# Kernel tuning notes

Hardware: AMD Instinct MI355X
Metric: run time of the kernel (lower is better)

Reference implementation:

```python
import jax, jax.numpy as jnp
import numpy as np

B, T, D = 2, 4096, 768
H = 12
HD = D // H  # 64
SCALE = 1.0 / np.sqrt(HD)


def setup_inputs() -> dict:
    key = jax.random.key(0)
    k1, k2, k3 = jax.random.split(key, 3)
    x = jax.random.normal(k1, (B, T, D), dtype=jnp.float32)
    W_qkv = jax.random.normal(k2, (D, 3 * D), dtype=jnp.float32) * (1.0 / np.sqrt(D))
    b_qkv = jnp.zeros((3 * D,), dtype=jnp.float32)
    W_out = jax.random.normal(k3, (D, D), dtype=jnp.float32) * (1.0 / np.sqrt(D))
    b_out = jnp.zeros((D,), dtype=jnp.float32)
    return {"x": x, "W_qkv": W_qkv, "b_qkv": b_qkv, "W_out": W_out, "b_out": b_out}


def reference(x, W_qkv, b_qkv, W_out, b_out):
    Bx, Tx, C = x.shape
    qkv = x @ W_qkv + b_qkv                                  # [B,T,3D]
    qkv = qkv.reshape(Bx, Tx, 3, H, HD).transpose(2, 0, 3, 1, 4)  # [3,B,H,T,hd]
    q, k, v = qkv[0], qkv[1], qkv[2]
    scores = jnp.einsum('bhqd,bhkd->bhqk', q, k) * SCALE      # [B,H,T,T]
    causal = jnp.tril(jnp.ones((Tx, Tx), dtype=bool))
    scores = jnp.where(causal[None, None], scores, -jnp.inf)
    attn = jax.nn.softmax(scores, axis=-1)
    out = jnp.einsum('bhqk,bhkd->bhqd', attn, v)              # [B,H,T,hd]
    out = out.transpose(0, 2, 1, 3).reshape(Bx, Tx, C)        # [B,T,D]
    return out @ W_out + b_out
```

## Files before the change

kernel.cpp:

```cpp
#include <hip/hip_runtime.h>
#include <cstdint>
#include <cstddef>

typedef _Float16 f16x8 __attribute__((ext_vector_type(8)));
typedef _Float16 f16x4 __attribute__((ext_vector_type(4)));
typedef float    f32x4 __attribute__((ext_vector_type(4)));

#define AS_GLOBAL __attribute__((address_space(1)))
#define AS_LDS    __attribute__((address_space(3)))

__device__ __forceinline__ void load16_to_lds(const _Float16* g, _Float16* l) {
    __builtin_amdgcn_global_load_lds((const AS_GLOBAL void*)g, (AS_LDS void*)l, 16, 0, 0);
}

#define BB   2
#define TT   4096
#define DD   768
#define NH   12
#define HDIM 64
#define D3   2304
#define SC2  (0.125f * 1.44269504088896f)

__global__ __launch_bounds__(256) void prep(const float* __restrict__ x,
                                            _Float16* __restrict__ Xh,
                                            const float* __restrict__ Wqkv,
                                            _Float16* __restrict__ Wqkvt,
                                            const float* __restrict__ Wout,
                                            _Float16* __restrict__ Wot) {
    const int bid = blockIdx.x, tid = threadIdx.x;
    if (bid < 6144) {
        const int i = bid * 1024 + tid * 4;
        float4 v = *(const float4*)(x + i);
        f16x4 h;
        h[0] = (_Float16)v.x; h[1] = (_Float16)v.y;
        h[2] = (_Float16)v.z; h[3] = (_Float16)v.w;
        *(f16x4*)(Xh + i) = h;
        return;
    }
    __shared__ float tile[32][33];
    const float* in; _Float16* out; int C, bx, by;
    if (bid < 7872) {
        const int t = bid - 6144;
        in = Wqkv; out = Wqkvt; C = 2304;
        bx = (t % 72) * 32; by = (t / 72) * 32;
    } else {
        const int t = bid - 7872;
        in = Wout; out = Wot; C = 768;
        bx = (t % 24) * 32; by = (t / 24) * 32;
    }
    const int R = 768;
    const int tx = tid & 31, ty = tid >> 5;
#pragma unroll
    for (int j = 0; j < 32; j += 8)
        tile[ty + j][tx] = in[(size_t)(by + ty + j) * C + bx + tx];
    __syncthreads();
#pragma unroll
    for (int j = 0; j < 32; j += 8)
        out[(size_t)(bx + ty + j) * R + by + tx] = (_Float16)tile[tx][ty + j];
}

template <typename OutT>
__device__ __forceinline__ void gemm_body(const _Float16* __restrict__ A,
                                          const _Float16* __restrict__ Bt,
                                          const float* __restrict__ bias, bool bias_row,
                                          OutT* __restrict__ C, int N, int K,
                                          int m0, int n0,
                                          _Float16* As, _Float16* Bs) {
    const int tid  = threadIdx.x;
    const int wave = tid >> 6, lane = tid & 63, quad = lane >> 4, l16 = lane & 15;
    const int wm = (wave & 1) * 64, wn = (wave >> 1) * 64;
    const int rowc = lane >> 3, part = lane & 7;

    f32x4 acc[4][4];
#pragma unroll
    for (int i = 0; i < 4; ++i)
#pragma unroll
        for (int n = 0; n < 4; ++n) acc[i][n] = f32x4{0.f, 0.f, 0.f, 0.f};

    for (int k0 = 0; k0 < K; k0 += 64) {
        __syncthreads();
#pragma unroll
        for (int cc = 0; cc < 4; ++cc) {
            const int ch = wave * 4 + cc;
            load16_to_lds(A  + (size_t)(m0 + ch * 8 + rowc) * K + k0 + part * 8,
                          As + ch * 512);
            load16_to_lds(Bt + (size_t)(n0 + ch * 8 + rowc) * K + k0 + part * 8,
                          Bs + ch * 512);
        }
        __syncthreads();
#pragma unroll
        for (int i = 0; i < 4; ++i) {
            f16x8 a0 = *(const f16x8*)(As + (wm + i * 16 + l16) * 64 + quad * 8);
            f16x8 a1 = *(const f16x8*)(As + (wm + i * 16 + l16) * 64 + 32 + quad * 8);
#pragma unroll
            for (int n = 0; n < 4; ++n) {
                f16x8 b0 = *(const f16x8*)(Bs + (wn + n * 16 + l16) * 64 + quad * 8);
                f16x8 b1 = *(const f16x8*)(Bs + (wn + n * 16 + l16) * 64 + 32 + quad * 8);
                acc[i][n] = __builtin_amdgcn_mfma_f32_16x16x32_f16(a0, b0, acc[i][n], 0, 0, 0);
                acc[i][n] = __builtin_amdgcn_mfma_f32_16x16x32_f16(a1, b1, acc[i][n], 0, 0, 0);
            }
        }
    }
#pragma unroll
    for (int i = 0; i < 4; ++i)
#pragma unroll
        for (int n = 0; n < 4; ++n)
#pragma unroll
            for (int r = 0; r < 4; ++r) {
                const int row = m0 + wm + i * 16 + quad * 4 + r;
                const int col = n0 + wn + n * 16 + l16;
                const float bv = bias_row ? bias[row] : bias[col];
                C[(size_t)row * N + col] = (OutT)(acc[i][n][r] + bv);
            }
}

__global__ __launch_bounds__(256) void gemm_qkv(const _Float16* __restrict__ Xh,
                                                const _Float16* __restrict__ Wqkvt,
                                                const float* __restrict__ bqkv,
                                                _Float16* __restrict__ QKh,
                                                _Float16* __restrict__ VtG) {
    __shared__ __align__(16) _Float16 As[128 * 64];
    __shared__ __align__(16) _Float16 Bs[128 * 64];
    const int bid = blockIdx.x;
    if (bid < 768) {
        const int bx = bid % 12, by = bid / 12;
        gemm_body<_Float16>(Xh, Wqkvt, bqkv, false, QKh, 1536, DD,
                            by * 128, bx * 128, As, Bs);
    } else {
        const int t = bid - 768;
        const int bx = t % 64, by = t / 64;
        gemm_body<_Float16>(Wqkvt + (size_t)1536 * DD, Xh, bqkv + 1536, true, VtG,
                            8192, DD, by * 128, bx * 128, As, Bs);
    }
}

__global__ __launch_bounds__(256) void gemm_out(const _Float16* __restrict__ A,
                                                const _Float16* __restrict__ Bt,
                                                const float* __restrict__ bias,
                                                float* __restrict__ C) {
    __shared__ __align__(16) _Float16 As[128 * 64];
    __shared__ __align__(16) _Float16 Bs[128 * 64];
    gemm_body<float>(A, Bt, bias, false, C, DD, DD,
                     (int)blockIdx.y * 128, (int)blockIdx.x * 128, As, Bs);
}

__global__ __launch_bounds__(256) void attn_kernel(const _Float16* __restrict__ qk,
                                                   const _Float16* __restrict__ vt,
                                                   _Float16* __restrict__ ao) {
    __shared__ __align__(16) _Float16 Ks[2][64 * 64];
    __shared__ __align__(16) _Float16 Vs[2][64 * 64];
    __shared__ __align__(16) _Float16 Ps[2][4][16 * 64];

    const int L    = blockIdx.x;
    const int xcd  = L & 7;
    const int r_   = L >> 3;
    const int gIdx = r_ >> 5;
    const int x    = r_ & 31;
    const int g    = gIdx * 8 + xcd;
    const int b = g / NH, h = g % NH;

    const int tid = threadIdx.x;
    const int wave = tid >> 6, lane = tid & 63, quad = lane >> 4, l16 = lane & 15;

    f16x8 ones;
#pragma unroll
    for (int j = 0; j < 8; ++j) ones[j] = (_Float16)1.0f;

    int vK[2], vV[2];
#pragma unroll
    for (int p = 0; p < 2; ++p) {
        const int j  = wave * 16 + p * 8 + (lane >> 3);
        const int sig = (j & 15) * 4 + (j >> 4);
        const int cdk = (lane & 7) ^ (j & 7);
        vK[p] = (b * TT + sig) * 1536 + DD + h * HDIM + cdk * 8;
        vV[p] = (h * HDIM + j) * 8192 + b * TT + cdk * 8;
    }
    auto stageK = [&](int buf, int k0) {
        const int kK = k0 * 1536;
#pragma unroll
        for (int p = 0; p < 2; ++p)
            load16_to_lds(qk + (vK[p] + kK), Ks[buf] + (wave * 16 + p * 8) * 64);
    };
    auto stageV = [&](int buf, int k0) {
#pragma unroll
        for (int p = 0; p < 2; ++p)
            load16_to_lds(vt + (vV[p] + k0), Vs[buf] + (wave * 16 + p * 8) * 64);
    };

    _Float16* const PsW = &Ps[0][wave][0];
    int pwo[4];
#pragma unroll
    for (int r = 0; r < 4; ++r) {
        const int row = quad * 4 + r;
        pwo[r] = row * 64 + (((l16 >> 1) ^ (row & 7)) * 8) + (l16 & 1) * 4;
    }
    int pro[2];
#pragma unroll
    for (int kh = 0; kh < 2; ++kh)
        pro[kh] = l16 * 64 + (((kh * 4 + quad) ^ (l16 & 7)) * 8);

    auto process = [&](int qt) {
        const int q0 = qt * 64;
        const int nkt = qt + 1;
        const int qrow = q0 + wave * 16 + quad * 4;
        f16x8 aq[2];
        {
            const int qoff = (b * TT + q0 + wave * 16 + l16) * 1536 + h * HDIM + quad * 8;
            const _Float16 sc = (_Float16)SC2;
            aq[0] = *(const f16x8*)(qk + qoff) * sc;
            aq[1] = *(const f16x8*)(qk + qoff + 32) * sc;
        }
        f32x4 o[4], lac;
#pragma unroll
        for (int n = 0; n < 4; ++n) o[n] = f32x4{0.f, 0.f, 0.f, 0.f};
        lac = f32x4{0.f, 0.f, 0.f, 0.f};

        auto pv = [&](int pbuf, int vbuf) {
#pragma unroll
            for (int kh = 0; kh < 2; ++kh) {
                f16x8 ap = *(const f16x8*)(PsW + pbuf * 4096 + pro[kh]);
                lac = __builtin_amdgcn_mfma_f32_16x16x32_f16(ap, ones, lac, 0, 0, 0);
#pragma unroll
                for (int n = 0; n < 4; ++n) {
                    const int posv = (kh * 4 + quad) ^ (l16 & 7);
                    f16x8 bv = *(const f16x8*)(Vs[vbuf] + (n * 16 + l16) * 64 + posv * 8);
                    o[n] = __builtin_amdgcn_mfma_f32_16x16x32_f16(ap, bv, o[n], 0, 0, 0);
                }
            }
        };

        __syncthreads();
        stageK(0, 0);
        int cur = 0;
        for (int kt = 0; kt < nkt; ++kt) {
            __syncthreads();
            if (kt + 1 < nkt) stageK(cur ^ 1, (kt + 1) * 64);
            stageV(cur, kt * 64);

            __builtin_amdgcn_s_setprio(1);
            f32x4 s[4];
#pragma unroll
            for (int n = 0; n < 4; ++n) s[n] = f32x4{0.f, 0.f, 0.f, 0.f};
#pragma unroll
            for (int kh = 0; kh < 2; ++kh)
#pragma unroll
                for (int n = 0; n < 4; ++n) {
                    const int pos = (kh * 4 + quad) ^ (l16 & 7);
                    f16x8 bk = *(const f16x8*)(Ks[cur] + (n * 16 + l16) * 64 + pos * 8);
                    s[n] = __builtin_amdgcn_mfma_f32_16x16x32_f16(aq[kh], bk, s[n], 0, 0, 0);
                }

            if (kt > 0) pv(cur ^ 1, cur ^ 1);
            __builtin_amdgcn_s_setprio(0);

            if (kt == nkt - 1) {
#pragma unroll
                for (int n = 0; n < 4; ++n) {
                    const int kg = kt * 64 + l16 * 4 + n;
#pragma unroll
                    for (int r = 0; r < 4; ++r)
                        if (kg > qrow + r) s[n][r] = -1e30f;
                }
            }

#pragma unroll
            for (int r = 0; r < 4; ++r) {
                f16x4 pk;
#pragma unroll
                for (int n = 0; n < 4; ++n)
                    pk[n] = (_Float16)__builtin_amdgcn_exp2f(s[n][r]);
                *(f16x4*)(PsW + cur * 4096 + pwo[r]) = pk;
            }
            cur ^= 1;
        }

        __syncthreads();
        pv(cur ^ 1, cur ^ 1);

#pragma unroll
        for (int r = 0; r < 4; ++r) {
            const float inv = 1.0f / lac[r];
            const int ooff = (b * TT + qrow + r) * DD + h * HDIM + l16;
#pragma unroll
            for (int n = 0; n < 4; ++n)
                ao[ooff + n * 16] = (_Float16)(o[n][r] * inv);
        }
    };

    process(63 - x);
    process(x);
}

extern "C" void kernel_launch(void* const* d_in, const int* in_sizes, int n_in,
                              void* d_out, int out_size, void* d_ws, size_t ws_size,
                              hipStream_t stream) {
    const float* x     = (const float*)d_in[0];
    const float* Wqkv  = (const float*)d_in[1];
    const float* bqkv  = (const float*)d_in[2];
    const float* Wout  = (const float*)d_in[3];
    const float* bout  = (const float*)d_in[4];
    float* out = (float*)d_out;

    char* ws = (char*)d_ws;
    _Float16* Xh    = (_Float16*)ws;  ws += (size_t)BB * TT * DD * 2;
    _Float16* Wqkvt = (_Float16*)ws;  ws += (size_t)D3 * DD * 2;
    _Float16* Wot   = (_Float16*)ws;  ws += (size_t)DD * DD * 2;
    _Float16* QKh   = (_Float16*)ws;  ws += (size_t)BB * TT * 1536 * 2;
    _Float16* VtG   = (_Float16*)ws;  ws += (size_t)DD * BB * TT * 2;
    _Float16* AOh   = (_Float16*)ws;  ws += (size_t)BB * TT * DD * 2;

    prep<<<8448, 256, 0, stream>>>(x, Xh, Wqkv, Wqkvt, Wout, Wot);

    gemm_qkv<<<1152, 256, 0, stream>>>(Xh, Wqkvt, bqkv, QKh, VtG);

    attn_kernel<<<768, 256, 0, stream>>>(QKh, VtG, AOh);

    gemm_out<<<dim3(DD / 128, (BB * TT) / 128), 256, 0, stream>>>(AOh, Wot, bout, out);
}
```

Baseline: 248.0 us.

## Launch one causal q-tile per attention block, longest-first, with single-buffered P

The attention kernel used to pair q-tiles (63-x and x) inside each block to balance causal work. It now launches 1536 blocks that each handle one q-tile, ordered so the heaviest tiles (largest qt) are dispatched first. The hardware scheduler then does the load balancing, and the blocks can spread across more CUs. The P staging buffer in LDS is also cut from two buffers to one per wave, which lowers LDS use and may raise occupancy. The cost is more block launch and prologue overhead, and the result depends on the dispatch order actually following blockIdx.

```diff
diff --git a/kernel.cpp b/kernel.cpp
--- a/kernel.cpp
+++ b/kernel.cpp
@@ -149,13 +149,13 @@
                                                    _Float16* __restrict__ ao) {
     __shared__ __align__(16) _Float16 Ks[2][64 * 64];
     __shared__ __align__(16) _Float16 Vs[2][64 * 64];
-    __shared__ __align__(16) _Float16 Ps[2][4][16 * 64];
+    __shared__ __align__(16) _Float16 Ps[4][16 * 64];
 
     const int L    = blockIdx.x;
     const int xcd  = L & 7;
     const int r_   = L >> 3;
-    const int gIdx = r_ >> 5;
-    const int x    = r_ & 31;
+    const int gIdx = r_ % 3;
+    const int qt   = 63 - r_ / 3;
     const int g    = gIdx * 8 + xcd;
     const int b = g / NH, h = g % NH;
 
@@ -187,108 +187,102 @@
             load16_to_lds(vt + (vV[p] + k0), Vs[buf] + (wave * 16 + p * 8) * 64);
     };
 
-    _Float16* const PsW = &Ps[0][wave][0];
-    int pwo[4];
+    _Float16* const PsW = &Ps[wave][0];
+    _Float16* pw[4];
 #pragma unroll
     for (int r = 0; r < 4; ++r) {
         const int row = quad * 4 + r;
-        pwo[r] = row * 64 + (((l16 >> 1) ^ (row & 7)) * 8) + (l16 & 1) * 4;
-    }
-    int pro[2];
+        pw[r] = PsW + row * 64 + (((l16 >> 1) ^ (row & 7)) * 8) + (l16 & 1) * 4;
+    }
+    const _Float16* pr[2];
 #pragma unroll
     for (int kh = 0; kh < 2; ++kh)
-        pro[kh] = l16 * 64 + (((kh * 4 + quad) ^ (l16 & 7)) * 8);
-
-    auto process = [&](int qt) {
-        const int q0 = qt * 64;
-        const int nkt = qt + 1;
-        const int qrow = q0 + wave * 16 + quad * 4;
-        f16x8 aq[2];
-        {
-            const int qoff = (b * TT + q0 + wave * 16 + l16) * 1536 + h * HDIM + quad * 8;
-            const _Float16 sc = (_Float16)SC2;
-            aq[0] = *(const f16x8*)(qk + qoff) * sc;
-            aq[1] = *(const f16x8*)(qk + qoff + 32) * sc;
-        }
-        f32x4 o[4], lac;
-#pragma unroll
-        for (int n = 0; n < 4; ++n) o[n] = f32x4{0.f, 0.f, 0.f, 0.f};
-        lac = f32x4{0.f, 0.f, 0.f, 0.f};
-
-        auto pv = [&](int pbuf, int vbuf) {
-#pragma unroll
-            for (int kh = 0; kh < 2; ++kh) {
-                f16x8 ap = *(const f16x8*)(PsW + pbuf * 4096 + pro[kh]);
-                lac = __builtin_amdgcn_mfma_f32_16x16x32_f16(ap, ones, lac, 0, 0, 0);
-#pragma unroll
-                for (int n = 0; n < 4; ++n) {
-                    const int posv = (kh * 4 + quad) ^ (l16 & 7);
-                    f16x8 bv = *(const f16x8*)(Vs[vbuf] + (n * 16 + l16) * 64 + posv * 8);
-                    o[n] = __builtin_amdgcn_mfma_f32_16x16x32_f16(ap, bv, o[n], 0, 0, 0);
-                }
-            }
-        };
-
+        pr[kh] = PsW + l16 * 64 + (((kh * 4 + quad) ^ (l16 & 7)) * 8);
+
+    const int q0 = qt * 64;
+    const int nkt = qt + 1;
+    const int qrow = q0 + wave * 16 + quad * 4;
+    f16x8 aq[2];
+    {
+        const int qoff = (b * TT + q0 + wave * 16 + l16) * 1536 + h * HDIM + quad * 8;
+        const _Float16 sc = (_Float16)SC2;
+        aq[0] = *(const f16x8*)(qk + qoff) * sc;
+        aq[1] = *(const f16x8*)(qk + qoff + 32) * sc;
+    }
+    f32x4 o[4], lac;
+#pragma unroll
+    for (int n = 0; n < 4; ++n) o[n] = f32x4{0.f, 0.f, 0.f, 0.f};
+    lac = f32x4{0.f, 0.f, 0.f, 0.f};
+
+    auto pv = [&](int vbuf) {
+#pragma unroll
+        for (int kh = 0; kh < 2; ++kh) {
+            f16x8 ap = *(const f16x8*)pr[kh];
+            lac = __builtin_amdgcn_mfma_f32_16x16x32_f16(ap, ones, lac, 0, 0, 0);
+#pragma unroll
+            for (int n = 0; n < 4; ++n) {
+                const int posv = (kh * 4 + quad) ^ (l16 & 7);
+                f16x8 bv = *(const f16x8*)(Vs[vbuf] + (n * 16 + l16) * 64 + posv * 8);
+                o[n] = __builtin_amdgcn_mfma_f32_16x16x32_f16(ap, bv, o[n], 0, 0, 0);
+            }
+        }
+    };
+
+    stageK(0, 0);
+    int cur = 0;
+    for (int kt = 0; kt < nkt; ++kt) {
         __syncthreads();
-        stageK(0, 0);
-        int cur = 0;
-        for (int kt = 0; kt < nkt; ++kt) {
-            __syncthreads();
-            if (kt + 1 < nkt) stageK(cur ^ 1, (kt + 1) * 64);
-            stageV(cur, kt * 64);
-
-            __builtin_amdgcn_s_setprio(1);
-            f32x4 s[4];
-#pragma unroll
-            for (int n = 0; n < 4; ++n) s[n] = f32x4{0.f, 0.f, 0.f, 0.f};
-#pragma unroll
-            for (int kh = 0; kh < 2; ++kh)
-#pragma unroll
-                for (int n = 0; n < 4; ++n) {
-                    const int pos = (kh * 4 + quad) ^ (l16 & 7);
-                    f16x8 bk = *(const f16x8*)(Ks[cur] + (n * 16 + l16) * 64 + pos * 8);
-                    s[n] = __builtin_amdgcn_mfma_f32_16x16x32_f16(aq[kh], bk, s[n], 0, 0, 0);
-                }
-
-            if (kt > 0) pv(cur ^ 1, cur ^ 1);
-            __builtin_amdgcn_s_setprio(0);
-
-            if (kt == nkt - 1) {
-#pragma unroll
-                for (int n = 0; n < 4; ++n) {
-                    const int kg = kt * 64 + l16 * 4 + n;
-#pragma unroll
-                    for (int r = 0; r < 4; ++r)
-                        if (kg > qrow + r) s[n][r] = -1e30f;
-                }
-            }
-
-#pragma unroll
-            for (int r = 0; r < 4; ++r) {
-                f16x4 pk;
-#pragma unroll
-                for (int n = 0; n < 4; ++n)
-                    pk[n] = (_Float16)__builtin_amdgcn_exp2f(s[n][r]);
-                *(f16x4*)(PsW + cur * 4096 + pwo[r]) = pk;
-            }
-            cur ^= 1;
-        }
-
-        __syncthreads();
-        pv(cur ^ 1, cur ^ 1);
+        if (kt + 1 < nkt) stageK(cur ^ 1, (kt + 1) * 64);
+        stageV(cur, kt * 64);
+
+        __builtin_amdgcn_s_setprio(1);
+        f32x4 s[4];
+#pragma unroll
+        for (int n = 0; n < 4; ++n) s[n] = f32x4{0.f, 0.f, 0.f, 0.f};
+#pragma unroll
+        for (int kh = 0; kh < 2; ++kh)
+#pragma unroll
+            for (int n = 0; n < 4; ++n) {
+                const int pos = (kh * 4 + quad) ^ (l16 & 7);
+                f16x8 bk = *(const f16x8*)(Ks[cur] + (n * 16 + l16) * 64 + pos * 8);
+                s[n] = __builtin_amdgcn_mfma_f32_16x16x32_f16(aq[kh], bk, s[n], 0, 0, 0);
+            }
+
+        if (kt > 0) pv(cur ^ 1);
+        __builtin_amdgcn_s_setprio(0);
+
+        if (kt == nkt - 1) {
+#pragma unroll
+            for (int n = 0; n < 4; ++n) {
+                const int kg = kt * 64 + l16 * 4 + n;
+#pragma unroll
+                for (int r = 0; r < 4; ++r)
+                    if (kg > qrow + r) s[n][r] = -1e30f;
+            }
+        }
 
 #pragma unroll
         for (int r = 0; r < 4; ++r) {
-            const float inv = 1.0f / lac[r];
-            const int ooff = (b * TT + qrow + r) * DD + h * HDIM + l16;
+            f16x4 pk;
 #pragma unroll
             for (int n = 0; n < 4; ++n)
-                ao[ooff + n * 16] = (_Float16)(o[n][r] * inv);
-        }
-    };
-
-    process(63 - x);
-    process(x);
+                pk[n] = (_Float16)__builtin_amdgcn_exp2f(s[n][r]);
+            *(f16x4*)pw[r] = pk;
+        }
+        cur ^= 1;
+    }
+
+    __syncthreads();
+    pv(cur ^ 1);
+
+#pragma unroll
+    for (int r = 0; r < 4; ++r) {
+        const float inv = 1.0f / lac[r];
+        const int ooff = (b * TT + qrow + r) * DD + h * HDIM + l16;
+#pragma unroll
+        for (int n = 0; n < 4; ++n)
+            ao[ooff + n * 16] = (_Float16)(o[n][r] * inv);
+    }
 }
 
 extern "C" void kernel_launch(void* const* d_in, const int* in_sizes, int n_in,
@@ -313,7 +307,7 @@
 
     gemm_qkv<<<1152, 256, 0, stream>>>(Xh, Wqkvt, bqkv, QKh, VtG);
 
-    attn_kernel<<<768, 256, 0, stream>>>(QKh, VtG, AOh);
+    attn_kernel<<<1536, 256, 0, stream>>>(QKh, VtG, AOh);
 
     gemm_out<<<dim3(DD / 128, (BB * TT) / 128), 256, 0, stream>>>(AOh, Wot, bout, out);
 }
```

Measured after the change: 246.6 us. Within noise of the previous version (-0.6%).
